# Kernel optimization log

Hardware: AMD Instinct MI355X
Metric: run time of the kernel (lower is better)

Reference implementation:

```python
import jax, jax.numpy as jnp
import numpy as np

N_NODES = 100000
N_EDGES = 1600000
F_IN = 128      # dataset.num_features
HID = 128       # hidden_dim (heads=1)
HID_POST = 128  # hidden_dim_post
EDGE_DIM = 16
N_CLASSES = 16
NEG_SLOPE = 0.2  # PyG GATConv default leaky_relu slope


def setup_inputs() -> dict:
    key = jax.random.key(0)
    ks = jax.random.split(key, 16)
    s = 0.1  # weight scale
    inp = {
        "x": jax.random.normal(ks[0], (N_NODES, F_IN), jnp.float32),
        "edge_attr": jax.random.normal(ks[1], (N_EDGES, EDGE_DIM), jnp.float32),
        "W0": jax.random.normal(ks[2], (F_IN, HID), jnp.float32) * s,
        "a_src0": jax.random.normal(ks[3], (HID,), jnp.float32) * s,
        "a_dst0": jax.random.normal(ks[4], (HID,), jnp.float32) * s,
        "We0": jax.random.normal(ks[5], (EDGE_DIM, HID), jnp.float32) * s,
        "a_e0": jax.random.normal(ks[6], (HID,), jnp.float32) * s,
        "b0": jnp.zeros((HID,), jnp.float32),
        "W1": jax.random.normal(ks[7], (HID, HID), jnp.float32) * s,
        "a_src1": jax.random.normal(ks[8], (HID,), jnp.float32) * s,
        "a_dst1": jax.random.normal(ks[9], (HID,), jnp.float32) * s,
        "We1": jax.random.normal(ks[10], (EDGE_DIM, HID), jnp.float32) * s,
        "a_e1": jax.random.normal(ks[11], (HID,), jnp.float32) * s,
        "b1": jnp.zeros((HID,), jnp.float32),
        "lin1_w": jax.random.normal(ks[12], (HID, HID_POST), jnp.float32) * s,
        "lin1_b": jnp.zeros((HID_POST,), jnp.float32),
        "lin2_w": jax.random.normal(ks[13], (HID_POST, N_CLASSES), jnp.float32) * s,
        "lin2_b": jnp.zeros((N_CLASSES,), jnp.float32),
        "edge_index": jax.random.randint(ks[14], (2, N_EDGES), 0, N_NODES, jnp.int64),
    }
    return inp


def gat_conv(x, src, dst, edge_attr, W, a_s, a_d, We, a_e, b):
    """PyG GATConv, heads=1, edge_dim set, add_self_loops=True (fill_value='mean')."""
    n = x.shape[0]
    xl = x @ W                       # [N, HID] shared lin for src/dst
    alpha_src_n = xl @ a_s           # [N]
    alpha_dst_n = xl @ a_d           # [N]
    # self loops: edge_attr filled with per-target-node mean of incoming edge_attr
    deg = jax.ops.segment_sum(jnp.ones(src.shape[0], x.dtype), dst, num_segments=n)
    ea_mean = jax.ops.segment_sum(edge_attr, dst, num_segments=n) / jnp.maximum(deg, 1.0)[:, None]
    loop = jnp.arange(n, dtype=src.dtype)
    src_f = jnp.concatenate([src, loop])
    dst_f = jnp.concatenate([dst, loop])
    ea_f = jnp.concatenate([edge_attr, ea_mean], axis=0)  # [E+N, EDGE_DIM]
    alpha_edge = (ea_f @ We) @ a_e                        # [E+N]
    alpha = jax.nn.leaky_relu(
        alpha_src_n[src_f] + alpha_dst_n[dst_f] + alpha_edge, NEG_SLOPE
    )
    # segment softmax over destination node (every node has its self loop -> nonempty)
    amax = jax.ops.segment_max(alpha, dst_f, num_segments=n)
    ex = jnp.exp(alpha - amax[dst_f])
    denom = jax.ops.segment_sum(ex, dst_f, num_segments=n)
    w = ex / denom[dst_f]                                 # [E+N]
    out = jax.ops.segment_sum(xl[src_f] * w[:, None], dst_f, num_segments=n)
    return out + b


def reference(x, edge_attr, W0, a_src0, a_dst0, We0, a_e0, b0,
              W1, a_src1, a_dst1, We1, a_e1, b1,
              lin1_w, lin1_b, lin2_w, lin2_b, edge_index):
    src, dst = edge_index[0], edge_index[1]
    # dropout layers are identity in eval mode
    h = jax.nn.relu(gat_conv(x, src, dst, edge_attr, W0, a_src0, a_dst0, We0, a_e0, b0))
    h = jax.nn.relu(gat_conv(h, src, dst, edge_attr, W1, a_src1, a_dst1, We1, a_e1, b1))
    h = jax.nn.relu(h @ lin1_w + lin1_b)
    logits = h @ lin2_w + lin2_b
    return jax.nn.log_softmax(logits, axis=-1)
```

## Files before the change

kernel.cpp:

```cpp
#include <hip/hip_runtime.h>
#include <math.h>

#define N_NODES 100000
#define N_EDGES 1600000
#define NEG 0.2f
#define MAXDEG 128
#define WPB 4

__device__ __forceinline__ float lrelu(float x){ return x > 0.f ? x : NEG*x; }
__device__ __forceinline__ unsigned short f2bf(float f){
  unsigned int u = __float_as_uint(f);
  u += 0x7FFFu + ((u >> 16) & 1u);
  return (unsigned short)(u >> 16);
}

__global__ __launch_bounds__(256) void k_deg(const int* __restrict__ dst, const float* __restrict__ eatt,
    const float* __restrict__ We0, const float* __restrict__ ae0,
    const float* __restrict__ We1, const float* __restrict__ ae1,
    int* __restrict__ deg, int* __restrict__ rank, float2* __restrict__ ae01){
  __shared__ float wea[32];
  int t = threadIdx.x;
  if (t < 32){
    const float* W = (t < 16) ? We0 : We1;
    const float* a = (t < 16) ? ae0 : ae1;
    int r = t & 15;
    float acc = 0.f;
    #pragma unroll
    for (int j=0;j<128;j++) acc += W[r*128+j]*a[j];
    wea[t] = acc;
  }
  __syncthreads();
  int e = blockIdx.x*256 + t;
  if (e >= N_EDGES) return;
  const float4* p = (const float4*)(eatt + (size_t)e*16);
  float4 a0=p[0], a1=p[1], a2=p[2], a3=p[3];
  float f0 = a0.x*wea[0] +a0.y*wea[1] +a0.z*wea[2] +a0.w*wea[3]
           + a1.x*wea[4] +a1.y*wea[5] +a1.z*wea[6] +a1.w*wea[7]
           + a2.x*wea[8] +a2.y*wea[9] +a2.z*wea[10]+a2.w*wea[11]
           + a3.x*wea[12]+a3.y*wea[13]+a3.z*wea[14]+a3.w*wea[15];
  float f1 = a0.x*wea[16]+a0.y*wea[17]+a0.z*wea[18]+a0.w*wea[19]
           + a1.x*wea[20]+a1.y*wea[21]+a1.z*wea[22]+a1.w*wea[23]
           + a2.x*wea[24]+a2.y*wea[25]+a2.z*wea[26]+a2.w*wea[27]
           + a3.x*wea[28]+a3.y*wea[29]+a3.z*wea[30]+a3.w*wea[31];
  rank[e] = atomicAdd(&deg[dst[e]], 1);
  ae01[e] = make_float2(f0, f1);
}

__global__ __launch_bounds__(256) void k_scan_a(const int* __restrict__ deg, int* __restrict__ incl, int* __restrict__ bsum){
  __shared__ int s[256];
  int t = threadIdx.x; int i = blockIdx.x*256 + t;
  int v = (i < N_NODES) ? deg[i] : 0;
  s[t] = v; __syncthreads();
  for (int off=1; off<256; off<<=1){
    int u = (t>=off)? s[t-off] : 0; __syncthreads();
    s[t] += u; __syncthreads();
  }
  if (i < N_NODES) incl[i] = s[t];
  if (t == 255) bsum[blockIdx.x] = s[t];
}
__global__ __launch_bounds__(512) void k_scan_b(const int* __restrict__ bsum, int* __restrict__ bexcl, int nb){
  __shared__ int s[512];
  int t = threadIdx.x;
  int v = (t<nb)? bsum[t] : 0;
  s[t] = v; __syncthreads();
  for (int off=1; off<512; off<<=1){
    int u = (t>=off)? s[t-off] : 0; __syncthreads();
    s[t] += u; __syncthreads();
  }
  if (t<nb) bexcl[t] = s[t]-v;
}
__global__ __launch_bounds__(256) void k_scan_c(const int* __restrict__ incl, const int* __restrict__ deg,
    const int* __restrict__ bexcl, int* __restrict__ rowptr){
  int i = blockIdx.x*256+threadIdx.x;
  if (i < N_NODES) rowptr[i] = incl[i] - deg[i] + bexcl[blockIdx.x];
  if (i == 0) rowptr[N_NODES] = N_EDGES;
}

__global__ __launch_bounds__(256) void k_fillf(const int* __restrict__ src, const int* __restrict__ dst,
     const int* __restrict__ rank, const float2* __restrict__ ae01,
     const int* __restrict__ rowptr, uint4* __restrict__ csr){
  int e = blockIdx.x*256+threadIdx.x;
  if (e >= N_EDGES) return;
  int d = dst[e];
  float2 ae = ae01[e];
  int pos = rowptr[d] + rank[e];
  csr[pos] = make_uint4((unsigned)src[e], __float_as_uint(ae.x), __float_as_uint(ae.y), 0u);
}

__global__ __launch_bounds__(256) void k_gemm(const float* __restrict__ X, const float* __restrict__ W,
    const float* __restrict__ bias, float* __restrict__ Y, unsigned short* __restrict__ Ybf,
    const float* __restrict__ a_s, const float* __restrict__ a_d,
    float* __restrict__ asrc, float* __restrict__ adst, int M, int relu){
  __shared__ float Xs[16][68];
  __shared__ float Ws[16][128];
  __shared__ float as_s[128], ad_s[128];
  int t = threadIdx.x;
  if (a_s && t < 128){ as_s[t] = a_s[t]; ad_s[t] = a_d[t]; }
  int row0 = blockIdx.x * 64;
  int tc = t & 15, tr = t >> 4;
  int c0 = tc*8, r0 = tr*4;
  int lr = t >> 2, lc = (t & 3) << 2;
  int wk = t >> 4, wc = (t & 15) * 8;
  float acc[4][8];
  #pragma unroll
  for (int i=0;i<4;i++)
    #pragma unroll
    for (int j=0;j<8;j++) acc[i][j]=0.f;
  int gr = row0 + lr;
  for (int k0=0; k0<128; k0+=16){
    float4 xv = make_float4(0.f,0.f,0.f,0.f);
    if (gr < M) xv = *(const float4*)(X + (size_t)gr*128 + k0 + lc);
    float4 wv0 = *(const float4*)(W + (size_t)(k0+wk)*128 + wc);
    float4 wv1 = *(const float4*)(W + (size_t)(k0+wk)*128 + wc + 4);
    __syncthreads();
    Xs[lc+0][lr]=xv.x; Xs[lc+1][lr]=xv.y; Xs[lc+2][lr]=xv.z; Xs[lc+3][lr]=xv.w;
    *(float4*)&Ws[wk][wc]   = wv0;
    *(float4*)&Ws[wk][wc+4] = wv1;
    __syncthreads();
    #pragma unroll
    for (int kk=0;kk<16;kk++){
      float4 a  = *(const float4*)&Xs[kk][r0];
      float4 b0 = *(const float4*)&Ws[kk][c0];
      float4 b1 = *(const float4*)&Ws[kk][c0+4];
      float av[4] = {a.x,a.y,a.z,a.w};
      float bv[8] = {b0.x,b0.y,b0.z,b0.w,b1.x,b1.y,b1.z,b1.w};
      #pragma unroll
      for (int i=0;i<4;i++)
        #pragma unroll
        for (int j=0;j<8;j++) acc[i][j] += av[i]*bv[j];
    }
  }
  #pragma unroll
  for (int i=0;i<4;i++){
    int r = row0 + r0 + i;
    float v[8];
    #pragma unroll
    for (int j=0;j<8;j++){
      float u = acc[i][j] + (bias ? bias[c0+j] : 0.f);
      v[j] = relu ? fmaxf(u, 0.f) : u;
    }
    if (r < M){
      if (Y){
        *(float4*)(Y + (size_t)r*128 + c0)     = make_float4(v[0],v[1],v[2],v[3]);
        *(float4*)(Y + (size_t)r*128 + c0 + 4) = make_float4(v[4],v[5],v[6],v[7]);
      }
      if (Ybf){
        uint4 pk;
        pk.x = (unsigned)f2bf(v[0]) | ((unsigned)f2bf(v[1])<<16);
        pk.y = (unsigned)f2bf(v[2]) | ((unsigned)f2bf(v[3])<<16);
        pk.z = (unsigned)f2bf(v[4]) | ((unsigned)f2bf(v[5])<<16);
        pk.w = (unsigned)f2bf(v[6]) | ((unsigned)f2bf(v[7])<<16);
        *(uint4*)(Ybf + (size_t)r*128 + c0) = pk;
      }
    }
    if (a_s){
      float s=0.f, d=0.f;
      #pragma unroll
      for (int j=0;j<8;j++){ s += v[j]*as_s[c0+j]; d += v[j]*ad_s[c0+j]; }
      #pragma unroll
      for (int off=1; off<16; off<<=1){ s += __shfl_xor(s,off); d += __shfl_xor(d,off); }
      if ((t & 15)==0 && r < M){ asrc[r]=s; adst[r]=d; }
    }
  }
}

__global__ __launch_bounds__(256) void k_agg(const int* __restrict__ rowptr, const uint4* __restrict__ csr,
    const float* __restrict__ asrc, const float* __restrict__ adst,
    const unsigned short* __restrict__ xlbf,
    const float* __restrict__ bias, float* __restrict__ out, int relu, int layer){
  int w = threadIdx.x >> 6;
  int lane = threadIdx.x & 63;
  int n = blockIdx.x * WPB + w;
  __shared__ float2 eb[WPB][MAXDEG];
  const char* xbase = (const char*)xlbf;
  int s0 = rowptr[n], s1 = rowptr[n+1];
  int deg = s1 - s0;
  float adst_n = adst[n];
  float m_edge = -1e30f;
  float sae = 0.f;
  for (int base=0; base<deg; base+=64){
    int i = base + lane;
    float a = -1e30f;
    if (i < deg){
      uint4 p4 = csr[s0 + i];
      int sx = (int)p4.x;
      float ae = __uint_as_float(layer ? p4.z : p4.y);
      float av = lrelu(asrc[sx] + adst_n + ae);
      if (i < MAXDEG) eb[w][i] = make_float2(av, __uint_as_float((unsigned)sx << 8));
      a = av;
      sae += ae;
    }
    for (int off=32; off; off>>=1) a = fmaxf(a, __shfl_xor(a, off));
    m_edge = fmaxf(m_edge, a);
  }
  for (int off=32; off; off>>=1) sae += __shfl_xor(sae, off);
  float aloop_n = sae / fmaxf((float)deg, 1.f);
  float al = lrelu(asrc[n] + adst_n + aloop_n);
  float m = fmaxf(m_edge, al);
  float p = 0.f;
  for (int i=lane; i<deg; i+=64){
    float av;
    if (i < MAXDEG) av = eb[w][i].x;
    else { uint4 p4 = csr[s0+i];
           av = lrelu(asrc[p4.x] + adst_n + __uint_as_float(layer ? p4.z : p4.y)); }
    float ev = __expf(av - m);
    if (i < MAXDEG) eb[w][i].x = ev;
    p += ev;
  }
  for (int off=32; off; off>>=1) p += __shfl_xor(p, off);
  float wl = __expf(al - m);
  float denom = p + wl;
  __syncthreads();
  int g = lane >> 4, cl = lane & 15;
  unsigned clb = (unsigned)(cl << 4);
  float acc[8];
  #pragma unroll
  for (int j=0;j<8;j++) acc[j]=0.f;
  if (g == 0){
    uint4 v = *(const uint4*)(xbase + (((unsigned)n << 8) + clb));
    unsigned int uu[4] = {v.x,v.y,v.z,v.w};
    #pragma unroll
    for (int q=0;q<4;q++){
      acc[2*q]   += wl * __uint_as_float(uu[q] << 16);
      acc[2*q+1] += wl * __uint_as_float(uu[q] & 0xFFFF0000u);
    }
  }
  if (deg <= MAXDEG){
    int dfull = deg & ~7;
    for (int i=0; i<dfull; i+=8){
      float2 e0 = eb[w][i+g];
      float2 e1 = eb[w][i+4+g];
      uint4 v0 = *(const uint4*)(xbase + (__float_as_uint(e0.y) + clb));
      uint4 v1 = *(const uint4*)(xbase + (__float_as_uint(e1.y) + clb));
      unsigned int uu0[4] = {v0.x,v0.y,v0.z,v0.w};
      unsigned int uu1[4] = {v1.x,v1.y,v1.z,v1.w};
      #pragma unroll
      for (int q=0;q<4;q++){
        acc[2*q]   += e0.x * __uint_as_float(uu0[q] << 16);
        acc[2*q+1] += e0.x * __uint_as_float(uu0[q] & 0xFFFF0000u);
      }
      #pragma unroll
      for (int q=0;q<4;q++){
        acc[2*q]   += e1.x * __uint_as_float(uu1[q] << 16);
        acc[2*q+1] += e1.x * __uint_as_float(uu1[q] & 0xFFFF0000u);
      }
    }
    for (int i=dfull; i<deg; i+=4){
      int idx = i + g;
      float we = 0.f; unsigned off = (unsigned)n << 8;
      if (idx < deg){ float2 e = eb[w][idx]; we = e.x; off = __float_as_uint(e.y); }
      uint4 v = *(const uint4*)(xbase + (off + clb));
      unsigned int uu[4] = {v.x,v.y,v.z,v.w};
      #pragma unroll
      for (int q=0;q<4;q++){
        acc[2*q]   += we * __uint_as_float(uu[q] << 16);
        acc[2*q+1] += we * __uint_as_float(uu[q] & 0xFFFF0000u);
      }
    }
  } else {
    for (int i=0; i<deg; i+=8){
      int idx0 = i + g, idx1 = i + 4 + g;
      int sx0 = n, sx1 = n; float we0 = 0.f, we1 = 0.f;
      if (idx0 < deg){
        if (idx0 < MAXDEG){ float2 e = eb[w][idx0]; we0 = e.x; sx0 = (int)(__float_as_uint(e.y) >> 8); }
        else { uint4 p4 = csr[s0+idx0]; sx0 = (int)p4.x;
               we0 = __expf(lrelu(asrc[sx0] + adst_n + __uint_as_float(layer ? p4.z : p4.y)) - m); }
      }
      if (idx1 < deg){
        if (idx1 < MAXDEG){ float2 e = eb[w][idx1]; we1 = e.x; sx1 = (int)(__float_as_uint(e.y) >> 8); }
        else { uint4 p4 = csr[s0+idx1]; sx1 = (int)p4.x;
               we1 = __expf(lrelu(asrc[sx1] + adst_n + __uint_as_float(layer ? p4.z : p4.y)) - m); }
      }
      uint4 v0 = *(const uint4*)(xbase + (((unsigned)sx0 << 8) + clb));
      uint4 v1 = *(const uint4*)(xbase + (((unsigned)sx1 << 8) + clb));
      unsigned int uu0[4] = {v0.x,v0.y,v0.z,v0.w};
      unsigned int uu1[4] = {v1.x,v1.y,v1.z,v1.w};
      #pragma unroll
      for (int q=0;q<4;q++){
        acc[2*q]   += we0 * __uint_as_float(uu0[q] << 16);
        acc[2*q+1] += we0 * __uint_as_float(uu0[q] & 0xFFFF0000u);
      }
      #pragma unroll
      for (int q=0;q<4;q++){
        acc[2*q]   += we1 * __uint_as_float(uu1[q] << 16);
        acc[2*q+1] += we1 * __uint_as_float(uu1[q] & 0xFFFF0000u);
      }
    }
  }
  #pragma unroll
  for (int j=0;j<8;j++){
    acc[j] += __shfl_xor(acc[j], 16);
    acc[j] += __shfl_xor(acc[j], 32);
  }
  if (lane < 16){
    float inv = 1.f/denom;
    float4 b0 = *(const float4*)(bias + cl*8);
    float4 b1 = *(const float4*)(bias + cl*8 + 4);
    float o[8];
    o[0]=acc[0]*inv+b0.x; o[1]=acc[1]*inv+b0.y; o[2]=acc[2]*inv+b0.z; o[3]=acc[3]*inv+b0.w;
    o[4]=acc[4]*inv+b1.x; o[5]=acc[5]*inv+b1.y; o[6]=acc[6]*inv+b1.z; o[7]=acc[7]*inv+b1.w;
    if (relu){
      #pragma unroll
      for (int j=0;j<8;j++) o[j]=fmaxf(o[j],0.f);
    }
    *(float4*)(out + (size_t)n*128 + cl*8)     = make_float4(o[0],o[1],o[2],o[3]);
    *(float4*)(out + (size_t)n*128 + cl*8 + 4) = make_float4(o[4],o[5],o[6],o[7]);
  }
}

__global__ __launch_bounds__(256) void k_mlp(const float* __restrict__ X, const float* __restrict__ W,
    const float* __restrict__ bias, const float* __restrict__ w2, const float* __restrict__ b2,
    float* __restrict__ out, int M){
  __shared__ float Xs[16][68];
  __shared__ float Ws[16][128];
  __shared__ float hs[64*132];
  __shared__ float b2s[16];
  int t = threadIdx.x;
  int row0 = blockIdx.x * 64;
  int tc = t & 15, tr = t >> 4;
  int c0 = tc*8, r0 = tr*4;
  int lr = t >> 2, lc = (t & 3) << 2;
  int wk = t >> 4, wc = (t & 15) * 8;
  float acc[4][8];
  #pragma unroll
  for (int i=0;i<4;i++)
    #pragma unroll
    for (int j=0;j<8;j++) acc[i][j]=0.f;
  int gr = row0 + lr;
  for (int k0=0; k0<128; k0+=16){
    float4 xv = make_float4(0.f,0.f,0.f,0.f);
    if (gr < M) xv = *(const float4*)(X + (size_t)gr*128 + k0 + lc);
    float4 wv0 = *(const float4*)(W + (size_t)(k0+wk)*128 + wc);
    float4 wv1 = *(const float4*)(W + (size_t)(k0+wk)*128 + wc + 4);
    __syncthreads();
    Xs[lc+0][lr]=xv.x; Xs[lc+1][lr]=xv.y; Xs[lc+2][lr]=xv.z; Xs[lc+3][lr]=xv.w;
    *(float4*)&Ws[wk][wc]   = wv0;
    *(float4*)&Ws[wk][wc+4] = wv1;
    __syncthreads();
    #pragma unroll
    for (int kk=0;kk<16;kk++){
      float4 a  = *(const float4*)&Xs[kk][r0];
      float4 b0 = *(const float4*)&Ws[kk][c0];
      float4 b1 = *(const float4*)&Ws[kk][c0+4];
      float av[4] = {a.x,a.y,a.z,a.w};
      float bv[8] = {b0.x,b0.y,b0.z,b0.w,b1.x,b1.y,b1.z,b1.w};
      #pragma unroll
      for (int i=0;i<4;i++)
        #pragma unroll
        for (int j=0;j<8;j++) acc[i][j] += av[i]*bv[j];
    }
  }
  __syncthreads();
  float* wflat = &Ws[0][0];
  #pragma unroll
  for (int i=0;i<2;i++) ((float4*)wflat)[t + i*256] = ((const float4*)w2)[t + i*256];
  if (t < 16) b2s[t] = b2[t];
  #pragma unroll
  for (int i=0;i<4;i++){
    float v[8];
    #pragma unroll
    for (int j=0;j<8;j++) v[j] = fmaxf(acc[i][j] + bias[c0+j], 0.f);
    int lrow = r0 + i;
    *(float4*)&hs[lrow*132 + c0]     = make_float4(v[0],v[1],v[2],v[3]);
    *(float4*)&hs[lrow*132 + c0 + 4] = make_float4(v[4],v[5],v[6],v[7]);
  }
  __syncthreads();
  int nl = t >> 2, cq = (t & 3) * 4;
  int n = row0 + nl;
  if (n < M){
    float a0=b2s[cq], a1=b2s[cq+1], a2=b2s[cq+2], a3=b2s[cq+3];
    const float* hp = &hs[nl*132];
    #pragma unroll 8
    for (int k=0;k<128;k++){
      float hv = hp[k];
      float4 w4 = *(const float4*)&wflat[k*16 + cq];
      a0 += hv*w4.x; a1 += hv*w4.y; a2 += hv*w4.z; a3 += hv*w4.w;
    }
    float m = fmaxf(fmaxf(a0,a1), fmaxf(a2,a3));
    m = fmaxf(m, __shfl_xor(m, 1));
    m = fmaxf(m, __shfl_xor(m, 2));
    float s = __expf(a0-m)+__expf(a1-m)+__expf(a2-m)+__expf(a3-m);
    s += __shfl_xor(s, 1);
    s += __shfl_xor(s, 2);
    float lse = m + __logf(s);
    *(float4*)(out + (size_t)n*16 + cq) = make_float4(a0-lse, a1-lse, a2-lse, a3-lse);
  }
}

extern "C" void kernel_launch(void* const* d_in, const int* in_sizes, int n_in,
                              void* d_out, int out_size, void* d_ws, size_t ws_size,
                              hipStream_t stream){
  const float* x    = (const float*)d_in[0];
  const float* eatt = (const float*)d_in[1];
  const float* W0   = (const float*)d_in[2];
  const float* as0  = (const float*)d_in[3];
  const float* ad0  = (const float*)d_in[4];
  const float* We0  = (const float*)d_in[5];
  const float* ae0  = (const float*)d_in[6];
  const float* b0   = (const float*)d_in[7];
  const float* W1   = (const float*)d_in[8];
  const float* as1  = (const float*)d_in[9];
  const float* ad1  = (const float*)d_in[10];
  const float* We1  = (const float*)d_in[11];
  const float* ae1  = (const float*)d_in[12];
  const float* b1   = (const float*)d_in[13];
  const float* l1w  = (const float*)d_in[14];
  const float* l1b  = (const float*)d_in[15];
  const float* l2w  = (const float*)d_in[16];
  const float* l2b  = (const float*)d_in[17];
  const int*   ei   = (const int*)d_in[18];
  const int* srcI = ei;
  const int* dstI = ei + N_EDGES;
  float* out = (float*)d_out;

  char* p = (char*)d_ws;
  auto alloc = [&](size_t bytes)->char*{ char* r = p; p += (bytes + 255) & ~255ull; return r; };
  unsigned short* Abf = (unsigned short*)alloc((size_t)N_NODES*128*2);
  float* B       = (float*)alloc((size_t)N_NODES*128*4);
  float* asrc    = (float*)alloc((size_t)N_NODES*4);
  float* adst    = (float*)alloc((size_t)N_NODES*4);
  int* deg     = (int*)alloc((size_t)N_NODES*4);
  int* rowptr  = (int*)alloc((size_t)(N_NODES+1)*4);
  uint4* csr   = (uint4*)alloc((size_t)N_EDGES*16);
  int* incl    = (int*)alloc((size_t)N_NODES*4);
  int* bsum    = (int*)alloc(512*4);
  int* bexcl   = (int*)alloc(512*4);
  float2* ae01 = (float2*)Abf;
  int*    rank = (int*)B;

  const int NB_E = (N_EDGES+255)/256;
  const int NB_N = (N_NODES+255)/256;
  const int NB_W = N_NODES/WPB;
  const int NB_G = (N_NODES+63)/64;

  hipMemsetAsync(deg,  0, (size_t)N_NODES*4, stream);
  k_deg   <<<NB_E,256,0,stream>>>(dstI, eatt, We0, ae0, We1, ae1, deg, rank, ae01);
  k_scan_a<<<NB_N,256,0,stream>>>(deg, incl, bsum);
  k_scan_b<<<1,  512,0,stream>>>(bsum, bexcl, NB_N);
  k_scan_c<<<NB_N,256,0,stream>>>(incl, deg, bexcl, rowptr);
  k_fillf <<<NB_E,256,0,stream>>>(srcI, dstI, rank, ae01, rowptr, csr);

  k_gemm <<<NB_G,256,0,stream>>>(x, W0, nullptr, nullptr, Abf, as0, ad0, asrc, adst, N_NODES, 0);
  k_agg  <<<NB_W,256,0,stream>>>(rowptr, csr, asrc, adst, Abf, b0, B, 1, 0);

  k_gemm <<<NB_G,256,0,stream>>>(B, W1, nullptr, nullptr, Abf, as1, ad1, asrc, adst, N_NODES, 0);
  k_agg  <<<NB_W,256,0,stream>>>(rowptr, csr, asrc, adst, Abf, b1, B, 1, 1);

  k_mlp  <<<NB_G,256,0,stream>>>(B, l1w, l1b, l2w, l2b, out, N_NODES);
}
```

Measured before the change: 639.8 us.

## Privatize degree atomics per XCC and compute MLP second layer in registers

Result: no change. 636.6 us (-0.5%).

```diff
diff --git a/kernel.cpp b/kernel.cpp
--- a/kernel.cpp
+++ b/kernel.cpp
@@ -13,11 +13,16 @@
   u += 0x7FFFu + ((u >> 16) & 1u);
   return (unsigned short)(u >> 16);
 }
+__device__ __forceinline__ unsigned xcc_id(){
+  unsigned x;
+  asm volatile("s_getreg_b32 %0, hwreg(HW_REG_XCC_ID)" : "=s"(x));
+  return x & 7u;
+}
 
 __global__ __launch_bounds__(256) void k_deg(const int* __restrict__ dst, const float* __restrict__ eatt,
     const float* __restrict__ We0, const float* __restrict__ ae0,
     const float* __restrict__ We1, const float* __restrict__ ae1,
-    int* __restrict__ deg, int* __restrict__ rank, float2* __restrict__ ae01){
+    int* __restrict__ deg8, int* __restrict__ rank, float2* __restrict__ ae01){
   __shared__ float wea[32];
   int t = threadIdx.x;
   if (t < 32){
@@ -30,6 +35,8 @@
     wea[t] = acc;
   }
   __syncthreads();
+  unsigned xcc = xcc_id();
+  int* mydeg = deg8 + (size_t)xcc * N_NODES;
   int e = blockIdx.x*256 + t;
   if (e >= N_EDGES) return;
   const float4* p = (const float4*)(eatt + (size_t)e*16);
@@ -42,14 +49,21 @@
            + a1.x*wea[20]+a1.y*wea[21]+a1.z*wea[22]+a1.w*wea[23]
            + a2.x*wea[24]+a2.y*wea[25]+a2.z*wea[26]+a2.w*wea[27]
            + a3.x*wea[28]+a3.y*wea[29]+a3.z*wea[30]+a3.w*wea[31];
-  rank[e] = atomicAdd(&deg[dst[e]], 1);
+  int r = atomicAdd(&mydeg[dst[e]], 1);
+  rank[e] = r | (int)(xcc << 24);
   ae01[e] = make_float2(f0, f1);
 }
 
-__global__ __launch_bounds__(256) void k_scan_a(const int* __restrict__ deg, int* __restrict__ incl, int* __restrict__ bsum){
+__global__ __launch_bounds__(256) void k_scan_a(const int* __restrict__ deg8, int* __restrict__ deg,
+    int* __restrict__ incl, int* __restrict__ bsum){
   __shared__ int s[256];
   int t = threadIdx.x; int i = blockIdx.x*256 + t;
-  int v = (i < N_NODES) ? deg[i] : 0;
+  int v = 0;
+  if (i < N_NODES){
+    #pragma unroll
+    for (int x=0;x<8;x++) v += deg8[(size_t)x*N_NODES + i];
+    deg[i] = v;
+  }
   s[t] = v; __syncthreads();
   for (int off=1; off<256; off<<=1){
     int u = (t>=off)? s[t-off] : 0; __syncthreads();
@@ -70,20 +84,31 @@
   if (t<nb) bexcl[t] = s[t]-v;
 }
 __global__ __launch_bounds__(256) void k_scan_c(const int* __restrict__ incl, const int* __restrict__ deg,
-    const int* __restrict__ bexcl, int* __restrict__ rowptr){
+    const int* __restrict__ bexcl, const int* __restrict__ deg8,
+    int* __restrict__ rowptr, int* __restrict__ rowptr8){
   int i = blockIdx.x*256+threadIdx.x;
-  if (i < N_NODES) rowptr[i] = incl[i] - deg[i] + bexcl[blockIdx.x];
+  if (i < N_NODES){
+    int base = incl[i] - deg[i] + bexcl[blockIdx.x];
+    rowptr[i] = base;
+    int run = base;
+    #pragma unroll
+    for (int x=0;x<8;x++){
+      rowptr8[(size_t)i*8 + x] = run;
+      run += deg8[(size_t)x*N_NODES + i];
+    }
+  }
   if (i == 0) rowptr[N_NODES] = N_EDGES;
 }
 
 __global__ __launch_bounds__(256) void k_fillf(const int* __restrict__ src, const int* __restrict__ dst,
      const int* __restrict__ rank, const float2* __restrict__ ae01,
-     const int* __restrict__ rowptr, uint4* __restrict__ csr){
+     const int* __restrict__ rowptr8, uint4* __restrict__ csr){
   int e = blockIdx.x*256+threadIdx.x;
   if (e >= N_EDGES) return;
   int d = dst[e];
+  unsigned rk = (unsigned)rank[e];
   float2 ae = ae01[e];
-  int pos = rowptr[d] + rank[e];
+  int pos = rowptr8[(size_t)d*8 + (rk >> 24)] + (int)(rk & 0xFFFFFFu);
   csr[pos] = make_uint4((unsigned)src[e], __float_as_uint(ae.x), __float_as_uint(ae.y), 0u);
 }
 
@@ -313,7 +338,6 @@
     float* __restrict__ out, int M){
   __shared__ float Xs[16][68];
   __shared__ float Ws[16][128];
-  __shared__ float hs[64*132];
   __shared__ float b2s[16];
   int t = threadIdx.x;
   int row0 = blockIdx.x * 64;
@@ -355,35 +379,44 @@
   #pragma unroll
   for (int i=0;i<2;i++) ((float4*)wflat)[t + i*256] = ((const float4*)w2)[t + i*256];
   if (t < 16) b2s[t] = b2[t];
+  float4 bba = *(const float4*)(bias + c0);
+  float4 bbb = *(const float4*)(bias + c0 + 4);
+  float bb[8] = {bba.x,bba.y,bba.z,bba.w,bbb.x,bbb.y,bbb.z,bbb.w};
+  #pragma unroll
+  for (int i=0;i<4;i++)
+    #pragma unroll
+    for (int j=0;j<8;j++) acc[i][j] = fmaxf(acc[i][j] + bb[j], 0.f);
+  __syncthreads();
+  float A0=0.f, A1=0.f, A2=0.f, A3=0.f;
+  int sl = (tc+1) & 15;
+  #pragma unroll 4
+  for (int s=0; s<16; s++){
+    int cls = (tc + s) & 15;
+    const float* wp = wflat + (size_t)c0*16 + cls;
+    float p0=0.f,p1=0.f,p2=0.f,p3=0.f;
+    #pragma unroll
+    for (int j=0;j<8;j++){
+      float wv = wp[j*16];
+      p0 += acc[0][j]*wv; p1 += acc[1][j]*wv; p2 += acc[2][j]*wv; p3 += acc[3][j]*wv;
+    }
+    A0+=p0; A1+=p1; A2+=p2; A3+=p3;
+    A0=__shfl(A0,sl,16); A1=__shfl(A1,sl,16); A2=__shfl(A2,sl,16); A3=__shfl(A3,sl,16);
+  }
+  float A[4] = {A0,A1,A2,A3};
+  float bcls = b2s[tc];
   #pragma unroll
   for (int i=0;i<4;i++){
-    float v[8];
-    #pragma unroll
-    for (int j=0;j<8;j++) v[j] = fmaxf(acc[i][j] + bias[c0+j], 0.f);
-    int lrow = r0 + i;
-    *(float4*)&hs[lrow*132 + c0]     = make_float4(v[0],v[1],v[2],v[3]);
-    *(float4*)&hs[lrow*132 + c0 + 4] = make_float4(v[4],v[5],v[6],v[7]);
-  }
-  __syncthreads();
-  int nl = t >> 2, cq = (t & 3) * 4;
-  int n = row0 + nl;
-  if (n < M){
-    float a0=b2s[cq], a1=b2s[cq+1], a2=b2s[cq+2], a3=b2s[cq+3];
-    const float* hp = &hs[nl*132];
-    #pragma unroll 8
-    for (int k=0;k<128;k++){
-      float hv = hp[k];
-      float4 w4 = *(const float4*)&wflat[k*16 + cq];
-      a0 += hv*w4.x; a1 += hv*w4.y; a2 += hv*w4.z; a3 += hv*w4.w;
-    }
-    float m = fmaxf(fmaxf(a0,a1), fmaxf(a2,a3));
-    m = fmaxf(m, __shfl_xor(m, 1));
-    m = fmaxf(m, __shfl_xor(m, 2));
-    float s = __expf(a0-m)+__expf(a1-m)+__expf(a2-m)+__expf(a3-m);
-    s += __shfl_xor(s, 1);
-    s += __shfl_xor(s, 2);
-    float lse = m + __logf(s);
-    *(float4*)(out + (size_t)n*16 + cq) = make_float4(a0-lse, a1-lse, a2-lse, a3-lse);
+    float v = A[i] + bcls;
+    float m = v;
+    #pragma unroll
+    for (int off=1; off<16; off<<=1) m = fmaxf(m, __shfl_xor(m, off, 16));
+    float ex = __expf(v - m);
+    float sum = ex;
+    #pragma unroll
+    for (int off=1; off<16; off<<=1) sum += __shfl_xor(sum, off, 16);
+    float lse = m + __logf(sum);
+    int r = row0 + r0 + i;
+    if (r < M) out[(size_t)r*16 + tc] = v - lse;
   }
 }
 
@@ -425,20 +458,23 @@
   int* incl    = (int*)alloc((size_t)N_NODES*4);
   int* bsum    = (int*)alloc(512*4);
   int* bexcl   = (int*)alloc(512*4);
-  float2* ae01 = (float2*)Abf;
-  int*    rank = (int*)B;
+  float2* ae01   = (float2*)Abf;
+  char*   Bc     = (char*)B;
+  int*    rank   = (int*)Bc;
+  int*    deg8   = (int*)(Bc + 6400000);
+  int*    rowptr8= (int*)(Bc + 6400000 + 3200000);
 
   const int NB_E = (N_EDGES+255)/256;
   const int NB_N = (N_NODES+255)/256;
   const int NB_W = N_NODES/WPB;
   const int NB_G = (N_NODES+63)/64;
 
-  hipMemsetAsync(deg,  0, (size_t)N_NODES*4, stream);
-  k_deg   <<<NB_E,256,0,stream>>>(dstI, eatt, We0, ae0, We1, ae1, deg, rank, ae01);
-  k_scan_a<<<NB_N,256,0,stream>>>(deg, incl, bsum);
+  hipMemsetAsync(deg8, 0, (size_t)8*N_NODES*4, stream);
+  k_deg   <<<NB_E,256,0,stream>>>(dstI, eatt, We0, ae0, We1, ae1, deg8, rank, ae01);
+  k_scan_a<<<NB_N,256,0,stream>>>(deg8, deg, incl, bsum);
   k_scan_b<<<1,  512,0,stream>>>(bsum, bexcl, NB_N);
-  k_scan_c<<<NB_N,256,0,stream>>>(incl, deg, bexcl, rowptr);
-  k_fillf <<<NB_E,256,0,stream>>>(srcI, dstI, rank, ae01, rowptr, csr);
+  k_scan_c<<<NB_N,256,0,stream>>>(incl, deg, bexcl, deg8, rowptr, rowptr8);
+  k_fillf <<<NB_E,256,0,stream>>>(srcI, dstI, rank, ae01, rowptr8, csr);
 
   k_gemm <<<NB_G,256,0,stream>>>(x, W0, nullptr, nullptr, Abf, as0, ad0, asrc, adst, N_NODES, 0);
   k_agg  <<<NB_W,256,0,stream>>>(rowptr, csr, asrc, adst, Abf, b0, B, 1, 0);
```
